# Optimization experiments

Measured on AMD Instinct MI355X. Metric: run time of the kernel, lower is better.

## Reference

```python
import jax, jax.numpy as jnp
import numpy as np

# Transformer_E (depth=1): Residual(PreNorm(MultiScaleRetention)) + Residual1(PreNorm1(FeedForward))
# MultiScaleRetention follows the standard RetNet parallel form, adapted to two inputs
# (Q from x, K/V from z) as implied by PreNorm passing both normed streams to fn.

B, S, DIM, HEADS, MLP = 16, 1024, 256, 4, 512
HEAD = DIM // HEADS  # per-head qkv size; v_dim = DIM
EPS = 1e-5           # torch LayerNorm/GroupNorm default eps


def _ln(x, w, b):
    mu = jnp.mean(x, -1, keepdims=True)
    var = jnp.mean((x - mu) ** 2, -1, keepdims=True)
    return (x - mu) * jax.lax.rsqrt(var + EPS) * w + b


def _decay_matrix():
    # RetNet gammas: 1 - exp(linspace(log(1/32), log(1/512), heads))
    gammas = 1.0 - jnp.exp(jnp.linspace(jnp.log(1.0 / 32.0), jnp.log(1.0 / 512.0), HEADS))
    n = jnp.arange(S)
    diff = (n[:, None] - n[None, :]).astype(jnp.float32)  # [S,S]
    causal = diff >= 0
    D = jnp.where(causal[None], gammas[:, None, None] ** diff[None], 0.0)  # [H,S,S]
    return D.astype(jnp.float32)


def setup_inputs() -> dict:
    key = jax.random.key(0)
    ks = jax.random.split(key, 9)
    s = 1.0 / DIM  # repo inits W as randn/hidden_size
    return {
        "x": jax.random.normal(ks[0], (B, S, DIM), jnp.float32),
        "y": jax.random.normal(ks[1], (B, S, DIM), jnp.float32),
        "ln1_w": jnp.ones((DIM,), jnp.float32),
        "ln1_b": jnp.zeros((DIM,), jnp.float32),
        "W_Q": jax.random.normal(ks[2], (HEADS, DIM, HEAD), jnp.float32) * s,
        "W_K": jax.random.normal(ks[3], (HEADS, DIM, HEAD), jnp.float32) * s,
        "W_V": jax.random.normal(ks[4], (HEADS, DIM, HEAD), jnp.float32) * s,
        "gn_w": jnp.ones((DIM,), jnp.float32),
        "gn_b": jnp.zeros((DIM,), jnp.float32),
        "W_G": jax.random.normal(ks[5], (DIM, DIM), jnp.float32) * s,
        "W_O": jax.random.normal(ks[6], (DIM, DIM), jnp.float32) * s,
        "ln2_w": jnp.ones((DIM,), jnp.float32),
        "ln2_b": jnp.zeros((DIM,), jnp.float32),
        "ff_w1": jax.random.normal(ks[7], (DIM, MLP), jnp.float32) * (DIM ** -0.5),
        "ff_b1": jnp.zeros((MLP,), jnp.float32),
        "ff_w2": jax.random.normal(ks[8], (MLP, DIM), jnp.float32) * (MLP ** -0.5),
        "ff_b2": jnp.zeros((DIM,), jnp.float32),
    }


def reference(x, y, ln1_w, ln1_b, W_Q, W_K, W_V, gn_w, gn_b, W_G, W_O,
              ln2_w, ln2_b, ff_w1, ff_b1, ff_w2, ff_b2):
    # PreNorm: x.real -> float (already real float32 here), shared LayerNorm on both streams
    xn = _ln(x, ln1_w, ln1_b)
    zn = _ln(y, ln1_w, ln1_b)

    # --- MultiScaleRetention (parallel form) ---
    Q = jnp.einsum('bsd,hde->bhse', xn, W_Q)
    K = jnp.einsum('bsd,hde->bhse', zn, W_K)
    V = jnp.einsum('bsd,hde->bhse', zn, W_V)
    D = _decay_matrix()                                       # [H,S,S] causal decay
    scores = jnp.einsum('bhne,bhme->bhnm', Q, K) * D[None]    # [B,H,S,S]
    Yh = jnp.einsum('bhnm,bhme->bhne', scores, V)             # [B,H,S,HEAD]

    # GroupNorm(heads, v_dim) applied token-wise: normalize each head slice
    mu = jnp.mean(Yh, -1, keepdims=True)
    var = jnp.mean((Yh - mu) ** 2, -1, keepdims=True)
    Yn = (Yh - mu) * jax.lax.rsqrt(var + EPS)
    Ycat = jnp.transpose(Yn, (0, 2, 1, 3)).reshape(x.shape[0], x.shape[1], DIM)
    Ycat = Ycat * gn_w + gn_b

    # swish gate + output projection
    g = xn @ W_G
    attn_out = ((g * jax.nn.sigmoid(g)) * Ycat) @ W_O

    x1 = attn_out + x                                         # Residual

    # --- FeedForward block (Residual1(PreNorm1(FFN))) ---
    x1n = _ln(x1, ln2_w, ln2_b)
    h = jax.nn.leaky_relu(x1n @ ff_w1 + ff_b1, negative_slope=0.01)
    ff = h @ ff_w2 + ff_b2
    return ff + x1
```

## Files before the change

### kernel.cpp

```cpp
#include <hip/hip_runtime.h>

typedef float f32x4 __attribute__((ext_vector_type(4)));
typedef short bf16x8 __attribute__((ext_vector_type(8)));

__device__ __forceinline__ unsigned short f2bf(float f) {
  unsigned int u = __builtin_bit_cast(unsigned int, f);
  u += 0x7fffu + ((u >> 16) & 1u);
  return (unsigned short)(u >> 16);
}
__device__ __forceinline__ float bf2f(unsigned short s) {
  unsigned int u = ((unsigned int)s) << 16;
  return __builtin_bit_cast(float, u);
}

__device__ __forceinline__ void gll16(const void* src, void* dst) {
  __builtin_amdgcn_global_load_lds((const __attribute__((address_space(1))) void*)src,
                                   (__attribute__((address_space(3))) void*)dst, 16, 0, 0);
}

__global__ __launch_bounds__(256) void prep(
    const float* __restrict__ x, const float* __restrict__ y,
    const float* __restrict__ ln1w, const float* __restrict__ ln1b,
    const float* __restrict__ WQ, const float* __restrict__ WK,
    const float* __restrict__ WV, const float* __restrict__ WG,
    const float* __restrict__ WO, const float* __restrict__ F1,
    const float* __restrict__ F2,
    unsigned short* __restrict__ XN, unsigned short* __restrict__ ZN,
    unsigned short* __restrict__ qg, unsigned short* __restrict__ kv,
    unsigned short* __restrict__ wo, unsigned short* __restrict__ f1,
    unsigned short* __restrict__ f2)
{
  __shared__ float tl[64 * 65];
  const int id = blockIdx.x;
  if (id < 8192) {
    const float* X = (id < 4096) ? x : y;
    unsigned short* Y = (id < 4096) ? XN : ZN;
    const int bid = id & 4095;
    const int lane = threadIdx.x & 63;
    const size_t row = (size_t)bid * 4 + (threadIdx.x >> 6);
    const float4 v = *reinterpret_cast<const float4*>(X + row * 256 + lane * 4);
    float s = v.x + v.y + v.z + v.w;
    #pragma unroll
    for (int off = 1; off < 64; off <<= 1) s += __shfl_xor(s, off);
    float mean = s * (1.0f / 256.0f);
    float dx = v.x - mean, dy = v.y - mean, dz = v.z - mean, dw = v.w - mean;
    float q = dx * dx + dy * dy + dz * dz + dw * dw;
    #pragma unroll
    for (int off = 1; off < 64; off <<= 1) q += __shfl_xor(q, off);
    float rstd = rsqrtf(q * (1.0f / 256.0f) + 1e-5f);
    float4 wv = *reinterpret_cast<const float4*>(ln1w + lane * 4);
    float4 bv = *reinterpret_cast<const float4*>(ln1b + lane * 4);
    ushort4 o;
    o.x = f2bf(dx * rstd * wv.x + bv.x);
    o.y = f2bf(dy * rstd * wv.y + bv.y);
    o.z = f2bf(dz * rstd * wv.z + bv.z);
    o.w = f2bf(dw * rstd * wv.w + bv.w);
    *reinterpret_cast<ushort4*>(Y + row * 256 + lane * 4) = o;
    return;
  }
  const int t = id - 8192;
  const float* srcp; unsigned short* dstp; int sstr, dstr;
  if (t < 48) {
    const float* W = (t < 16) ? WQ : (t < 32) ? WK : WV;
    unsigned short* D = (t < 16) ? qg : kv;
    int tt = t & 15, h = tt >> 2, dt = tt & 3;
    int nof = (t >= 32) ? 256 : 0;
    srcp = W + ((size_t)(h * 256 + dt * 64)) * 64; sstr = 64;
    dstp = D + ((size_t)(nof + h * 64)) * 256 + dt * 64; dstr = 256;
  } else if (t < 64) {
    int tt = t - 48, r = tt >> 2, cc = tt & 3;
    srcp = WG + (size_t)(r * 64) * 256 + cc * 64; sstr = 256;
    dstp = qg + (size_t)(256 + cc * 64) * 256 + r * 64; dstr = 256;
  } else if (t < 80) {
    int tt = t - 64, r = tt >> 2, cc = tt & 3;
    srcp = WO + (size_t)(r * 64) * 256 + cc * 64; sstr = 256;
    dstp = wo + (size_t)(cc * 64) * 256 + r * 64; dstr = 256;
  } else if (t < 112) {
    int tt = t - 80, r = tt >> 3, cc = tt & 7;
    srcp = F1 + (size_t)(r * 64) * 512 + cc * 64; sstr = 512;
    dstp = f1 + (size_t)(cc * 64) * 256 + r * 64; dstr = 256;
  } else {
    int tt = t - 112, r = tt >> 2, cc = tt & 3;
    srcp = F2 + (size_t)(r * 64) * 256 + cc * 64; sstr = 256;
    dstp = f2 + (size_t)(cc * 64) * 512 + r * 64; dstr = 512;
  }
  {
    const int row = threadIdx.x >> 2, cq = threadIdx.x & 3;
    #pragma unroll
    for (int q = 0; q < 4; ++q) {
      int col = cq * 16 + q * 4;
      float4 v = *reinterpret_cast<const float4*>(srcp + (size_t)row * sstr + col);
      tl[(col + 0) * 65 + row] = v.x;
      tl[(col + 1) * 65 + row] = v.y;
      tl[(col + 2) * 65 + row] = v.z;
      tl[(col + 3) * 65 + row] = v.w;
    }
    __syncthreads();
    const int c2 = threadIdx.x >> 2, kq = threadIdx.x & 3;
    bf16x8 v0, v1;
    #pragma unroll
    for (int k = 0; k < 8; ++k) {
      v0[k] = (short)f2bf(tl[c2 * 65 + kq * 16 + k]);
      v1[k] = (short)f2bf(tl[c2 * 65 + kq * 16 + 8 + k]);
    }
    *reinterpret_cast<bf16x8*>(dstp + (size_t)c2 * dstr + kq * 16) = v0;
    *reinterpret_cast<bf16x8*>(dstp + (size_t)c2 * dstr + kq * 16 + 8) = v1;
  }
}

template<int MODE>
__global__ __launch_bounds__(256) void gemm128(
    const unsigned short* __restrict__ A0, const unsigned short* __restrict__ A1,
    const unsigned short* __restrict__ B0, const unsigned short* __restrict__ B1,
    unsigned short* __restrict__ o0, unsigned short* __restrict__ o1,
    unsigned short* __restrict__ o2, unsigned short* __restrict__ o3,
    const float* __restrict__ bias)
{
  __shared__ __align__(16) char sA[2][16384];
  __shared__ __align__(16) char sB[2][16384];
  const int tid = threadIdx.x, lane = tid & 63, w = tid >> 6;
  const int z = (MODE == 0) ? blockIdx.z : 0;
  const unsigned short* A = (MODE == 0 && z) ? A1 : A0;
  const unsigned short* Bw = (MODE == 0 && z) ? B1 : B0;
  const int flat = blockIdx.x;
  const int c = flat & 7, jj = flat >> 3;
  const int m0 = (c * 16 + (jj & 15)) * 128;
  const int n0 = (jj >> 4) * 128;
  const int wr = (w >> 1) * 64, wc = (w & 1) * 64;
  const char* Ab = (const char*)A + (size_t)m0 * 512;
  const char* Bb = (const char*)Bw + (size_t)n0 * 512;
  const int srow = lane >> 3;
  const int soff = 16 * ((lane & 7) ^ srow);
  f32x4 acc[4][4] = {};

  auto stage = [&](int bufi, int kt) {
    #pragma unroll
    for (int p = 0; p < 4; ++p) {
      int row = p * 32 + w * 8 + srow;
      gll16(Ab + (size_t)row * 512 + kt + soff, &sA[bufi][p * 4096 + w * 1024]);
      gll16(Bb + (size_t)row * 512 + kt + soff, &sB[bufi][p * 4096 + w * 1024]);
    }
  };

  stage(0, 0);
  asm volatile("s_waitcnt vmcnt(0)" ::: "memory");
  __syncthreads();
  int buf = 0;
  for (int kt = 0; kt < 512; kt += 128) {
    if (kt + 128 < 512) stage(buf ^ 1, kt + 128);
    #pragma unroll
    for (int kk = 0; kk < 2; ++kk) {
      const int ib = kk * 64 + ((lane >> 4) * 16);
      bf16x8 af[4], bfr[4];
      #pragma unroll
      for (int rf = 0; rf < 4; ++rf) {
        int row = wr + rf * 16 + (lane & 15);
        af[rf] = *reinterpret_cast<const bf16x8*>(&sA[buf][row * 128 + (ib ^ ((row & 7) << 4))]);
      }
      #pragma unroll
      for (int cf = 0; cf < 4; ++cf) {
        int row = wc + cf * 16 + (lane & 15);
        bfr[cf] = *reinterpret_cast<const bf16x8*>(&sB[buf][row * 128 + (ib ^ ((row & 7) << 4))]);
      }
      #pragma unroll
      for (int rf = 0; rf < 4; ++rf)
        #pragma unroll
        for (int cf = 0; cf < 4; ++cf)
          acc[rf][cf] = __builtin_amdgcn_mfma_f32_16x16x32_bf16(af[rf], bfr[cf], acc[rf][cf], 0, 0, 0);
    }
    asm volatile("s_waitcnt vmcnt(0)" ::: "memory");
    __syncthreads();
    buf ^= 1;
  }

  if constexpr (MODE == 0) {
    if (z == 1 && n0 >= 256) {
      char* sT = (char*)sA;
      #pragma unroll
      for (int rf = 0; rf < 4; ++rf) {
        #pragma unroll
        for (int cf = 0; cf < 4; ++cf) {
          const int colL = wc + cf * 16 + (lane & 15);
          const int tokL = wr + rf * 16 + ((lane >> 4) * 4);
          f32x4 v = acc[rf][cf];
          #pragma unroll
          for (int j = 0; j < 4; ++j)
            *reinterpret_cast<unsigned short*>(
                sT + colL * 256 + (((tokL + j) * 2) ^ ((colL & 15) << 4))) = f2bf(v[j]);
        }
      }
      __syncthreads();
      const int b10 = m0 & 1023, bb = m0 >> 10;
      #pragma unroll
      for (int it = 0; it < 8; ++it) {
        int idx = it * 256 + tid, colL = idx >> 4, t16 = idx & 15;
        uint4 vv = *reinterpret_cast<uint4*>(sT + colL * 256 + ((t16 * 16) ^ ((colL & 15) << 4)));
        int vc = (n0 - 256) + colL, hh = vc >> 6, e = vc & 63;
        int bh = bb * 4 + hh;
        *reinterpret_cast<uint4*>(o3 + ((((size_t)bh * 64 + e) << 10) + b10 + t16 * 8)) = vv;
      }
      return;
    }
  }

  #pragma unroll
  for (int rf = 0; rf < 4; ++rf) {
    #pragma unroll
    for (int cf = 0; cf < 4; ++cf) {
      const int r0 = m0 + wr + rf * 16 + ((lane >> 4) * 4);
      const int col = n0 + wc + cf * 16 + (lane & 15);
      f32x4 v = acc[rf][cf];
      if constexpr (MODE == 1) {
        float bc = bias[col];
        #pragma unroll
        for (int j = 0; j < 4; ++j) {
          float t = v[j] + bc;
          o0[(size_t)(r0 + j) * 512 + col] = f2bf(t >= 0.0f ? t : 0.01f * t);
        }
      } else {
        if (z == 0) {
          const bool lowhalf = (n0 + wc + cf * 16) < 256;
          unsigned short* dst = lowhalf ? o0 : o1;
          int ccol = col & 255;
          #pragma unroll
          for (int j = 0; j < 4; ++j) dst[(size_t)(r0 + j) * 256 + ccol] = f2bf(v[j]);
        } else {
          #pragma unroll
          for (int j = 0; j < 4; ++j) o2[(size_t)(r0 + j) * 256 + col] = f2bf(v[j]);
        }
      }
    }
  }
}

template<int EPI>
__global__ __launch_bounds__(256) void gemm_nt(
    const unsigned short* __restrict__ A, const unsigned short* __restrict__ Bw,
    int K, unsigned short* __restrict__ o0,
    const float* __restrict__ bias, const float* __restrict__ resid,
    float* __restrict__ of)
{
  __shared__ __align__(16) char sA[2][16384];
  __shared__ __align__(16) char sB[2][8192];
  const int tid = threadIdx.x, lane = tid & 63, w = tid >> 6;
  const int flat = blockIdx.x + gridDim.x * blockIdx.y;
  const int c = flat & 7, jj = flat >> 3;
  const int m0 = (c * 16 + (jj & 15)) * 128;
  const int n0 = (jj >> 4) * 64;
  const int wr = (w >> 1) * 64, wc = (w & 1) * 32;
  const int K2 = K * 2;
  const char* Ab = (const char*)A + (size_t)m0 * K2;
  const char* Bb = (const char*)Bw + (size_t)n0 * K2;
  const int srow = lane >> 3;
  const int soff = 16 * ((lane & 7) ^ srow);
  f32x4 acc[4][2] = {};

  auto stage = [&](int bufi, int kt) {
    #pragma unroll
    for (int p = 0; p < 4; ++p) {
      int row = p * 32 + w * 8 + srow;
      gll16(Ab + (size_t)row * K2 + kt + soff, &sA[bufi][p * 4096 + w * 1024]);
    }
    #pragma unroll
    for (int p = 0; p < 2; ++p) {
      int row = p * 32 + w * 8 + srow;
      gll16(Bb + (size_t)row * K2 + kt + soff, &sB[bufi][p * 4096 + w * 1024]);
    }
  };

  stage(0, 0);
  asm volatile("s_waitcnt vmcnt(0)" ::: "memory");
  __syncthreads();
  int buf = 0;
  for (int kt = 0; kt < K2; kt += 128) {
    if (kt + 128 < K2) stage(buf ^ 1, kt + 128);
    #pragma unroll
    for (int kk = 0; kk < 2; ++kk) {
      const int ib = kk * 64 + ((lane >> 4) * 16);
      bf16x8 af[4], bfr[2];
      #pragma unroll
      for (int rf = 0; rf < 4; ++rf) {
        int row = wr + rf * 16 + (lane & 15);
        af[rf] = *reinterpret_cast<const bf16x8*>(&sA[buf][row * 128 + (ib ^ ((row & 7) << 4))]);
      }
      #pragma unroll
      for (int cf = 0; cf < 2; ++cf) {
        int row = wc + cf * 16 + (lane & 15);
        bfr[cf] = *reinterpret_cast<const bf16x8*>(&sB[buf][row * 128 + (ib ^ ((row & 7) << 4))]);
      }
      #pragma unroll
      for (int rf = 0; rf < 4; ++rf)
        #pragma unroll
        for (int cf = 0; cf < 2; ++cf)
          acc[rf][cf] = __builtin_amdgcn_mfma_f32_16x16x32_bf16(af[rf], bfr[cf], acc[rf][cf], 0, 0, 0);
    }
    asm volatile("s_waitcnt vmcnt(0)" ::: "memory");
    __syncthreads();
    buf ^= 1;
  }

  #pragma unroll
  for (int rf = 0; rf < 4; ++rf) {
    #pragma unroll
    for (int cf = 0; cf < 2; ++cf) {
      const int r0 = m0 + wr + rf * 16 + ((lane >> 4) * 4);
      const int col = n0 + wc + cf * 16 + (lane & 15);
      f32x4 v = acc[rf][cf];
      if constexpr (EPI == 3) {
        float bc = bias[col];
        #pragma unroll
        for (int j = 0; j < 4; ++j) {
          float t = v[j] + bc;
          o0[(size_t)(r0 + j) * 512 + col] = f2bf(t >= 0.0f ? t : 0.01f * t);
        }
      } else {
        float bc = bias[col];
        #pragma unroll
        for (int j = 0; j < 4; ++j) {
          size_t idx = (size_t)(r0 + j) * 256 + col;
          of[idx] = v[j] + bc + resid[idx];
        }
      }
    }
  }
}

__global__ __launch_bounds__(256) void gemm_wo_ln(
    const unsigned short* __restrict__ AY, const unsigned short* __restrict__ WoT,
    const float* __restrict__ x, const float* __restrict__ ln2w,
    const float* __restrict__ ln2b,
    float* __restrict__ X1, unsigned short* __restrict__ X1N)
{
  __shared__ __align__(16) char sA[2][4096];
  __shared__ __align__(16) char sB[2][32768];
  __shared__ float redS[32][4], redQ[32][4];
  const int tid = threadIdx.x, lane = tid & 63, w = tid >> 6;
  const int id = blockIdx.x;
  const int c = id & 7, j5 = id >> 3;
  const int m0 = (c * 64 + j5) * 32;
  const char* Ab = (const char*)AY + (size_t)m0 * 512;
  const char* Bb = (const char*)WoT;
  const int srow = lane >> 3;
  const int soff = 16 * ((lane & 7) ^ srow);
  f32x4 acc[2][4] = {};

  auto stage = [&](int bufi, int kt) {
    {
      int row = w * 8 + srow;
      gll16(Ab + (size_t)row * 512 + kt + soff, &sA[bufi][w * 1024]);
    }
    #pragma unroll
    for (int p = 0; p < 8; ++p) {
      int row = w * 64 + p * 8 + srow;
      gll16(Bb + (size_t)row * 512 + kt + soff, &sB[bufi][w * 8192 + p * 1024]);
    }
  };

  stage(0, 0);
  asm volatile("s_waitcnt vmcnt(0)" ::: "memory");
  __syncthreads();
  int buf = 0;
  for (int kt = 0; kt < 512; kt += 128) {
    if (kt + 128 < 512) stage(buf ^ 1, kt + 128);
    #pragma unroll
    for (int kk = 0; kk < 2; ++kk) {
      const int ib = kk * 64 + ((lane >> 4) * 16);
      bf16x8 af[2], bfr[4];
      #pragma unroll
      for (int mf = 0; mf < 2; ++mf) {
        int row = mf * 16 + (lane & 15);
        af[mf] = *reinterpret_cast<const bf16x8*>(&sA[buf][row * 128 + (ib ^ ((row & 7) << 4))]);
      }
      #pragma unroll
      for (int nf = 0; nf < 4; ++nf) {
        int row = w * 64 + nf * 16 + (lane & 15);
        bfr[nf] = *reinterpret_cast<const bf16x8*>(&sB[buf][row * 128 + (ib ^ ((row & 7) << 4))]);
      }
      #pragma unroll
      for (int mf = 0; mf < 2; ++mf)
        #pragma unroll
        for (int nf = 0; nf < 4; ++nf)
          acc[mf][nf] = __builtin_amdgcn_mfma_f32_16x16x32_bf16(af[mf], bfr[nf], acc[mf][nf], 0, 0, 0);
    }
    asm volatile("s_waitcnt vmcnt(0)" ::: "memory");
    __syncthreads();
    buf ^= 1;
  }

  #pragma unroll
  for (int mf = 0; mf < 2; ++mf) {
    #pragma unroll
    for (int j = 0; j < 4; ++j) {
      const int rowg = m0 + mf * 16 + ((lane >> 4) * 4) + j;
      float s = 0.0f, q = 0.0f;
      #pragma unroll
      for (int nf = 0; nf < 4; ++nf) {
        const int col = w * 64 + nf * 16 + (lane & 15);
        float v = acc[mf][nf][j] + x[(size_t)rowg * 256 + col];
        acc[mf][nf][j] = v;
        s += v; q += v * v;
      }
      #pragma unroll
      for (int off = 1; off < 16; off <<= 1) { s += __shfl_xor(s, off); q += __shfl_xor(q, off); }
      if ((lane & 15) == 0) {
        int rl = mf * 16 + ((lane >> 4) * 4) + j;
        redS[rl][w] = s; redQ[rl][w] = q;
      }
    }
  }
  __syncthreads();
  #pragma unroll
  for (int mf = 0; mf < 2; ++mf) {
    #pragma unroll
    for (int j = 0; j < 4; ++j) {
      const int rl = mf * 16 + ((lane >> 4) * 4) + j;
      const int rowg = m0 + rl;
      float sm = redS[rl][0] + redS[rl][1] + redS[rl][2] + redS[rl][3];
      float sq = redQ[rl][0] + redQ[rl][1] + redQ[rl][2] + redQ[rl][3];
      float mean = sm * (1.0f / 256.0f);
      float var = sq * (1.0f / 256.0f) - mean * mean;
      float rstd = rsqrtf(var + 1e-5f);
      #pragma unroll
      for (int nf = 0; nf < 4; ++nf) {
        const int col = w * 64 + nf * 16 + (lane & 15);
        float v = acc[mf][nf][j];
        X1[(size_t)rowg * 256 + col] = v;
        X1N[(size_t)rowg * 256 + col] = f2bf((v - mean) * rstd * ln2w[col] + ln2b[col]);
      }
    }
  }
}

__global__ __launch_bounds__(256) void attn_ret(
    const unsigned short* __restrict__ Qb, const unsigned short* __restrict__ Kb,
    const unsigned short* __restrict__ Vt, const unsigned short* __restrict__ Gb,
    const float* __restrict__ gnw, const float* __restrict__ gnb,
    unsigned short* __restrict__ AY)
{
  __shared__ __align__(16) char sK[2][8192];
  __shared__ __align__(16) char sV[2][8192];
  __shared__ __align__(16) char sP[8192];
  const int tid = threadIdx.x, lane = tid & 63, w = tid >> 6;
  const int id = blockIdx.x;
  const int c = id & 7, jid = id >> 3;
  const int bh = c * 8 + (jid & 7);
  const int g = jid >> 3;
  const int qt = (g < 4) ? (15 - g) : (g < 8) ? (11 - g) : (g < 12) ? g : (g - 12);
  const int b = bh >> 2, h = bh & 3;

  const float la = logf(1.0f / 32.0f), lb = logf(1.0f / 512.0f);
  const float gamma = 1.0f - expf(la + (lb - la) * ((float)h * (1.0f / 3.0f)));
  const float lg = log2f(gamma);

  const char* Qg = (const char*)Qb
      + ((size_t)(b * 1024 + qt * 64 + w * 16 + (lane & 15))) * 512 + h * 128 + (lane >> 4) * 16;
  const bf16x8 aq0 = *reinterpret_cast<const bf16x8*>(Qg);
  const bf16x8 aq1 = *reinterpret_cast<const bf16x8*>(Qg + 64);

  const int nl = w * 16 + (lane & 15);
  const int hi = lane >> 4;
  float Rt = exp2f((float)(qt * 64 + nl) * lg);
  const float g64i = exp2f(-64.0f * lg);
  float Mq[4], Mc[4];
  #pragma unroll
  for (int j = 0; j < 4; ++j) Mq[j] = exp2f(-(float)(hi * 4 + j) * lg);
  #pragma unroll
  for (int cf = 0; cf < 4; ++cf) Mc[cf] = exp2f(-(float)(cf * 16) * lg);

  const char* Kg = (const char*)Kb + ((size_t)(b * 1024)) * 512 + h * 128;
  const char* Vg = (const char*)Vt + ((size_t)bh * 64) * 2048;
  const int srow = lane >> 3;
  const int soff = 16 * ((lane & 7) ^ srow);

  auto stage = [&](int bufi, int t) {
    const char* kb = Kg + (size_t)(t * 64) * 512;
    const char* vb = Vg + (size_t)(t * 64) * 2;
    #pragma unroll
    for (int p = 0; p < 2; ++p) {
      int row = p * 32 + w * 8 + srow;
      gll16(kb + (size_t)row * 512 + soff, &sK[bufi][p * 4096 + w * 1024]);
      gll16(vb + (size_t)row * 2048 + soff, &sV[bufi][p * 4096 + w * 1024]);
    }
  };

  stage(0, 0);
  f32x4 o[4] = {};
  asm volatile("s_waitcnt vmcnt(0)" ::: "memory");
  __syncthreads();
  int buf = 0;

  for (int t = 0; t <= qt; ++t) {
    if (t < qt) stage(buf ^ 1, t + 1);

    f32x4 s4[4] = {};
    #pragma unroll
    for (int kk = 0; kk < 2; ++kk) {
      const int ib = kk * 64 + (hi * 16);
      const bf16x8 aq = kk ? aq1 : aq0;
      #pragma unroll
      for (int cf = 0; cf < 4; ++cf) {
        int kr = cf * 16 + (lane & 15);
        bf16x8 bk = *reinterpret_cast<const bf16x8*>(&sK[buf][kr * 128 + (ib ^ ((kr & 7) << 4))]);
        s4[cf] = __builtin_amdgcn_mfma_f32_16x16x32_bf16(bk, aq, s4[cf], 0, 0, 0);
      }
    }

    const bool diag = (t == qt);
    #pragma unroll
    for (int cf = 0; cf < 4; ++cf) {
      const float rm = Rt * Mc[cf];
      ushort4 pk;
      {
        float p0 = s4[cf][0] * (rm * Mq[0]);
        float p1 = s4[cf][1] * (rm * Mq[1]);
        float p2 = s4[cf][2] * (rm * Mq[2]);
        float p3 = s4[cf][3] * (rm * Mq[3]);
        if (diag) {
          const int mlb = cf * 16 + hi * 4;
          if (nl - (mlb + 0) < 0) p0 = 0.0f;
          if (nl - (mlb + 1) < 0) p1 = 0.0f;
          if (nl - (mlb + 2) < 0) p2 = 0.0f;
          if (nl - (mlb + 3) < 0) p3 = 0.0f;
        }
        pk.x = f2bf(p0); pk.y = f2bf(p1); pk.z = f2bf(p2); pk.w = f2bf(p3);
      }
      *reinterpret_cast<ushort4*>(
          sP + nl * 128 + ((cf * 32 + hi * 8) ^ ((nl & 7) << 4))) = pk;
    }

    #pragma unroll
    for (int kk = 0; kk < 2; ++kk) {
      const int ib = kk * 64 + (hi * 16);
      int pr = w * 16 + (lane & 15);
      bf16x8 ap = *reinterpret_cast<const bf16x8*>(sP + pr * 128 + (ib ^ ((pr & 7) << 4)));
      #pragma unroll
      for (int cf = 0; cf < 4; ++cf) {
        int vr = cf * 16 + (lane & 15);
        bf16x8 bv = *reinterpret_cast<const bf16x8*>(&sV[buf][vr * 128 + (ib ^ ((vr & 7) << 4))]);
        o[cf] = __builtin_amdgcn_mfma_f32_16x16x32_bf16(ap, bv, o[cf], 0, 0, 0);
      }
    }
    Rt *= g64i;

    asm volatile("s_waitcnt vmcnt(0)" ::: "memory");
    __syncthreads();
    buf ^= 1;
  }

  const int nloc_b = w * 16 + (hi * 4);
  float gw[4], gb[4];
  #pragma unroll
  for (int cf = 0; cf < 4; ++cf) {
    int col = h * 64 + cf * 16 + (lane & 15);
    gw[cf] = gnw[col]; gb[cf] = gnb[col];
  }
  const int tokb = b * 1024 + qt * 64 + nloc_b;
  #pragma unroll
  for (int j = 0; j < 4; ++j) {
    float sm = 0.0f, sq = 0.0f;
    #pragma unroll
    for (int cf = 0; cf < 4; ++cf) { float xv = o[cf][j]; sm += xv; sq += xv * xv; }
    #pragma unroll
    for (int off = 1; off < 16; off <<= 1) { sm += __shfl_xor(sm, off); sq += __shfl_xor(sq, off); }
    float mean = sm * (1.0f / 64.0f);
    float var = sq * (1.0f / 64.0f) - mean * mean;
    float rstd = rsqrtf(var + 1e-5f);
    size_t tok = (size_t)(tokb + j);
    #pragma unroll
    for (int cf = 0; cf < 4; ++cf) {
      int col = h * 64 + cf * 16 + (lane & 15);
      float yn = (o[cf][j] - mean) * rstd * gw[cf] + gb[cf];
      float gv = bf2f(Gb[tok * 256 + col]);
      float sg = gv / (1.0f + expf(-gv));
      AY[tok * 256 + col] = f2bf(yn * sg);
    }
  }
}

extern "C" void kernel_launch(void* const* d_in, const int* in_sizes, int n_in,
                              void* d_out, int out_size, void* d_ws, size_t ws_size,
                              hipStream_t stream) {
  const float* x     = (const float*)d_in[0];
  const float* y     = (const float*)d_in[1];
  const float* ln1_w = (const float*)d_in[2];
  const float* ln1_b = (const float*)d_in[3];
  const float* W_Q   = (const float*)d_in[4];
  const float* W_K   = (const float*)d_in[5];
  const float* W_V   = (const float*)d_in[6];
  const float* gn_w  = (const float*)d_in[7];
  const float* gn_b  = (const float*)d_in[8];
  const float* W_G   = (const float*)d_in[9];
  const float* W_O   = (const float*)d_in[10];
  const float* ln2_w = (const float*)d_in[11];
  const float* ln2_b = (const float*)d_in[12];
  const float* ff_w1 = (const float*)d_in[13];
  const float* ff_b1 = (const float*)d_in[14];
  const float* ff_w2 = (const float*)d_in[15];
  const float* ff_b2 = (const float*)d_in[16];

  char* ws = (char*)d_ws;
  const size_t MB = 1048576;
  unsigned short* XN  = (unsigned short*)(ws + 0 * MB);
  unsigned short* ZN  = (unsigned short*)(ws + 8 * MB);
  unsigned short* QB  = (unsigned short*)(ws + 16 * MB);
  unsigned short* KB  = (unsigned short*)(ws + 24 * MB);
  unsigned short* VT  = (unsigned short*)(ws + 32 * MB);
  unsigned short* GB  = (unsigned short*)(ws + 40 * MB);
  unsigned short* WQG = (unsigned short*)(ws + 48 * MB);
  unsigned short* WKV = (unsigned short*)(ws + 48 * MB + 262144);
  unsigned short* WOp = (unsigned short*)(ws + 48 * MB + 524288);
  unsigned short* F1p = (unsigned short*)(ws + 48 * MB + 655360);
  unsigned short* F2p = (unsigned short*)(ws + 48 * MB + 917504);
  float*          X1  = (float*)(ws + 16 * MB);
  unsigned short* X1N = (unsigned short*)(ws + 32 * MB);
  unsigned short* H   = (unsigned short*)(ws + 0 * MB);
  unsigned short* AY  = ZN;
  float* out = (float*)d_out;

  prep<<<8336, 256, 0, stream>>>(x, y, ln1_w, ln1_b, W_Q, W_K, W_V, W_G, W_O,
                                 ff_w1, ff_w2, XN, ZN, WQG, WKV, WOp, F1p, F2p);
  gemm128<0><<<dim3(512, 1, 2), 256, 0, stream>>>(XN, ZN, WQG, WKV, QB, GB, KB, VT, nullptr);
  attn_ret<<<1024, 256, 0, stream>>>(QB, KB, VT, GB, gn_w, gn_b, AY);
  gemm_wo_ln<<<512, 256, 0, stream>>>(AY, WOp, x, ln2_w, ln2_b, X1, X1N);
  gemm128<1><<<dim3(512, 1, 1), 256, 0, stream>>>(X1N, nullptr, F1p, nullptr, H, nullptr, nullptr, nullptr, ff_b1);
  gemm_nt<4><<<dim3(4, 128), 256, 0, stream>>>(H, F2p, 512, nullptr, ff_b2, X1, out);
}
```

Baseline: 92.43 us.

## Pair complementary query tiles per block to share K/V staging in retention

Each retention block now processes two query tiles, qlo and 15-qlo, against the same double-buffered K/V stream instead of one tile. Each staged K/V tile is reused by both query tiles, and every block does the same amount of causal work, so the grid shrinks from 1024 to 512 blocks. The aim is to halve K/V global traffic and remove the load imbalance of triangular causal tiles. In exchange the block holds two sets of Q fragments and accumulators, which raises register pressure, and there are fewer blocks to hide latency.

Measured after the change: 95.64 us. 1.03x slower.

```diff
diff --git a/kernel.cpp b/kernel.cpp
--- a/kernel.cpp
+++ b/kernel.cpp
@@ -444,22 +444,28 @@
   const int id = blockIdx.x;
   const int c = id & 7, jid = id >> 3;
   const int bh = c * 8 + (jid & 7);
-  const int g = jid >> 3;
-  const int qt = (g < 4) ? (15 - g) : (g < 8) ? (11 - g) : (g < 12) ? g : (g - 12);
+  const int gg = jid >> 3;
+  const int gmap[8] = {7, 0, 6, 1, 5, 2, 4, 3};
+  const int qlo = gmap[gg], qhi = 15 - qlo;
   const int b = bh >> 2, h = bh & 3;
 
   const float la = logf(1.0f / 32.0f), lb = logf(1.0f / 512.0f);
   const float gamma = 1.0f - expf(la + (lb - la) * ((float)h * (1.0f / 3.0f)));
   const float lg = log2f(gamma);
 
-  const char* Qg = (const char*)Qb
-      + ((size_t)(b * 1024 + qt * 64 + w * 16 + (lane & 15))) * 512 + h * 128 + (lane >> 4) * 16;
-  const bf16x8 aq0 = *reinterpret_cast<const bf16x8*>(Qg);
-  const bf16x8 aq1 = *reinterpret_cast<const bf16x8*>(Qg + 64);
+  const char* QgH = (const char*)Qb
+      + ((size_t)(b * 1024 + qhi * 64 + w * 16 + (lane & 15))) * 512 + h * 128 + (lane >> 4) * 16;
+  const bf16x8 aqh0 = *reinterpret_cast<const bf16x8*>(QgH);
+  const bf16x8 aqh1 = *reinterpret_cast<const bf16x8*>(QgH + 64);
+  const char* QgL = (const char*)Qb
+      + ((size_t)(b * 1024 + qlo * 64 + w * 16 + (lane & 15))) * 512 + h * 128 + (lane >> 4) * 16;
+  const bf16x8 aql0 = *reinterpret_cast<const bf16x8*>(QgL);
+  const bf16x8 aql1 = *reinterpret_cast<const bf16x8*>(QgL + 64);
 
   const int nl = w * 16 + (lane & 15);
   const int hi = lane >> 4;
-  float Rt = exp2f((float)(qt * 64 + nl) * lg);
+  float RtH = exp2f((float)(qhi * 64 + nl) * lg);
+  float RtL = exp2f((float)(qlo * 64 + nl) * lg);
   const float g64i = exp2f(-64.0f * lg);
   float Mq[4], Mc[4];
   #pragma unroll
@@ -484,19 +490,17 @@
   };
 
   stage(0, 0);
-  f32x4 o[4] = {};
+  f32x4 oH[4] = {}, oL[4] = {};
   asm volatile("s_waitcnt vmcnt(0)" ::: "memory");
   __syncthreads();
   int buf = 0;
 
-  for (int t = 0; t <= qt; ++t) {
-    if (t < qt) stage(buf ^ 1, t + 1);
-
+  auto body = [&](const bf16x8& a0, const bf16x8& a1, float Rt, bool diag, f32x4* o) {
     f32x4 s4[4] = {};
     #pragma unroll
     for (int kk = 0; kk < 2; ++kk) {
       const int ib = kk * 64 + (hi * 16);
-      const bf16x8 aq = kk ? aq1 : aq0;
+      const bf16x8 aq = kk ? a1 : a0;
       #pragma unroll
       for (int cf = 0; cf < 4; ++cf) {
         int kr = cf * 16 + (lane & 15);
@@ -504,30 +508,25 @@
         s4[cf] = __builtin_amdgcn_mfma_f32_16x16x32_bf16(bk, aq, s4[cf], 0, 0, 0);
       }
     }
-
-    const bool diag = (t == qt);
     #pragma unroll
     for (int cf = 0; cf < 4; ++cf) {
       const float rm = Rt * Mc[cf];
       ushort4 pk;
-      {
-        float p0 = s4[cf][0] * (rm * Mq[0]);
-        float p1 = s4[cf][1] * (rm * Mq[1]);
-        float p2 = s4[cf][2] * (rm * Mq[2]);
-        float p3 = s4[cf][3] * (rm * Mq[3]);
-        if (diag) {
-          const int mlb = cf * 16 + hi * 4;
-          if (nl - (mlb + 0) < 0) p0 = 0.0f;
-          if (nl - (mlb + 1) < 0) p1 = 0.0f;
-          if (nl - (mlb + 2) < 0) p2 = 0.0f;
-          if (nl - (mlb + 3) < 0) p3 = 0.0f;
-        }
-        pk.x = f2bf(p0); pk.y = f2bf(p1); pk.z = f2bf(p2); pk.w = f2bf(p3);
-      }
+      float p0 = s4[cf][0] * (rm * Mq[0]);
+      float p1 = s4[cf][1] * (rm * Mq[1]);
+      float p2 = s4[cf][2] * (rm * Mq[2]);
+      float p3 = s4[cf][3] * (rm * Mq[3]);
+      if (diag) {
+        const int mlb = cf * 16 + hi * 4;
+        if (nl - (mlb + 0) < 0) p0 = 0.0f;
+        if (nl - (mlb + 1) < 0) p1 = 0.0f;
+        if (nl - (mlb + 2) < 0) p2 = 0.0f;
+        if (nl - (mlb + 3) < 0) p3 = 0.0f;
+      }
+      pk.x = f2bf(p0); pk.y = f2bf(p1); pk.z = f2bf(p2); pk.w = f2bf(p3);
       *reinterpret_cast<ushort4*>(
           sP + nl * 128 + ((cf * 32 + hi * 8) ^ ((nl & 7) << 4))) = pk;
     }
-
     #pragma unroll
     for (int kk = 0; kk < 2; ++kk) {
       const int ib = kk * 64 + (hi * 16);
@@ -540,8 +539,16 @@
         o[cf] = __builtin_amdgcn_mfma_f32_16x16x32_bf16(ap, bv, o[cf], 0, 0, 0);
       }
     }
-    Rt *= g64i;
-
+  };
+
+  for (int t = 0; t <= qhi; ++t) {
+    if (t < qhi) stage(buf ^ 1, t + 1);
+    body(aqh0, aqh1, RtH, t == qhi, oH);
+    RtH *= g64i;
+    if (t <= qlo) {
+      body(aql0, aql1, RtL, t == qlo, oL);
+      RtL *= g64i;
+    }
     asm volatile("s_waitcnt vmcnt(0)" ::: "memory");
     __syncthreads();
     buf ^= 1;
@@ -554,27 +561,31 @@
     int col = h * 64 + cf * 16 + (lane & 15);
     gw[cf] = gnw[col]; gb[cf] = gnb[col];
   }
-  const int tokb = b * 1024 + qt * 64 + nloc_b;
-  #pragma unroll
-  for (int j = 0; j < 4; ++j) {
-    float sm = 0.0f, sq = 0.0f;
-    #pragma unroll
-    for (int cf = 0; cf < 4; ++cf) { float xv = o[cf][j]; sm += xv; sq += xv * xv; }
-    #pragma unroll
-    for (int off = 1; off < 16; off <<= 1) { sm += __shfl_xor(sm, off); sq += __shfl_xor(sq, off); }
-    float mean = sm * (1.0f / 64.0f);
-    float var = sq * (1.0f / 64.0f) - mean * mean;
-    float rstd = rsqrtf(var + 1e-5f);
-    size_t tok = (size_t)(tokb + j);
-    #pragma unroll
-    for (int cf = 0; cf < 4; ++cf) {
-      int col = h * 64 + cf * 16 + (lane & 15);
-      float yn = (o[cf][j] - mean) * rstd * gw[cf] + gb[cf];
-      float gv = bf2f(Gb[tok * 256 + col]);
-      float sg = gv / (1.0f + expf(-gv));
-      AY[tok * 256 + col] = f2bf(yn * sg);
-    }
-  }
+  auto gnout = [&](const f32x4* o, int qt) {
+    const int tokb = b * 1024 + qt * 64 + nloc_b;
+    #pragma unroll
+    for (int j = 0; j < 4; ++j) {
+      float sm = 0.0f, sq = 0.0f;
+      #pragma unroll
+      for (int cf = 0; cf < 4; ++cf) { float xv = o[cf][j]; sm += xv; sq += xv * xv; }
+      #pragma unroll
+      for (int off = 1; off < 16; off <<= 1) { sm += __shfl_xor(sm, off); sq += __shfl_xor(sq, off); }
+      float mean = sm * (1.0f / 64.0f);
+      float var = sq * (1.0f / 64.0f) - mean * mean;
+      float rstd = rsqrtf(var + 1e-5f);
+      size_t tok = (size_t)(tokb + j);
+      #pragma unroll
+      for (int cf = 0; cf < 4; ++cf) {
+        int col = h * 64 + cf * 16 + (lane & 15);
+        float yn = (o[cf][j] - mean) * rstd * gw[cf] + gb[cf];
+        float gv = bf2f(Gb[tok * 256 + col]);
+        float sg = gv / (1.0f + expf(-gv));
+        AY[tok * 256 + col] = f2bf(yn * sg);
+      }
+    }
+  };
+  gnout(oH, qhi);
+  gnout(oL, qlo);
 }
 
 extern "C" void kernel_launch(void* const* d_in, const int* in_sizes, int n_in,
@@ -620,7 +631,7 @@
   prep<<<8336, 256, 0, stream>>>(x, y, ln1_w, ln1_b, W_Q, W_K, W_V, W_G, W_O,
                                  ff_w1, ff_w2, XN, ZN, WQG, WKV, WOp, F1p, F2p);
   gemm128<0><<<dim3(512, 1, 2), 256, 0, stream>>>(XN, ZN, WQG, WKV, QB, GB, KB, VT, nullptr);
-  attn_ret<<<1024, 256, 0, stream>>>(QB, KB, VT, GB, gn_w, gn_b, AY);
+  attn_ret<<<512, 256, 0, stream>>>(QB, KB, VT, GB, gn_w, gn_b, AY);
   gemm_wo_ln<<<512, 256, 0, stream>>>(AY, WOp, x, ln2_w, ln2_b, X1, X1N);
   gemm128<1><<<dim3(512, 1, 1), 256, 0, stream>>>(X1N, nullptr, F1p, nullptr, H, nullptr, nullptr, nullptr, ff_b1);
   gemm_nt<4><<<dim3(4, 128), 256, 0, stream>>>(H, F2p, 512, nullptr, ff_b2, X1, out);
```
